# Kernel optimization log

Hardware: AMD Instinct MI355X
Metric: run time of the kernel (lower is better)

Reference implementation:

```python
import jax, jax.numpy as jnp
import numpy as np


def _grid_sample_3d(vol, grid):
    """Trilinear 3D grid_sample, zero padding, align_corners=False (torch default).

    vol:  [B, C, D, H, W]
    grid: [B, P, 3] normalized coords in [-1, 1]; grid[...,0]->W axis,
          grid[...,1]->H axis, grid[...,2]->D axis (torch convention).
    returns [B, C, P]
    """
    B, C, D, H, W = vol.shape
    x = (grid[..., 0] + 1.0) * (W * 0.5) - 0.5
    y = (grid[..., 1] + 1.0) * (H * 0.5) - 0.5
    z = (grid[..., 2] + 1.0) * (D * 0.5) - 0.5
    x0, y0, z0 = jnp.floor(x), jnp.floor(y), jnp.floor(z)
    gather = jax.vmap(lambda v, zz, yy, xx: v[:, zz, yy, xx])  # per-batch gather -> [C, P]
    out = jnp.zeros((B, C, x.shape[1]), vol.dtype)
    for dz in (0.0, 1.0):
        for dy in (0.0, 1.0):
            for dx in (0.0, 1.0):
                xi, yi, zi = x0 + dx, y0 + dy, z0 + dz
                w = (1.0 - jnp.abs(x - xi)) * (1.0 - jnp.abs(y - yi)) * (1.0 - jnp.abs(z - zi))
                valid = (xi >= 0) & (xi < W) & (yi >= 0) & (yi < H) & (zi >= 0) & (zi < D)
                xc = jnp.clip(xi, 0, W - 1).astype(jnp.int32)
                yc = jnp.clip(yi, 0, H - 1).astype(jnp.int32)
                zc = jnp.clip(zi, 0, D - 1).astype(jnp.int32)
                vals = gather(vol, zc, yc, xc)  # [B, C, P]
                out = out + vals * jnp.where(valid, w, 0.0)[:, None, :]
    return out


def _offset_grid(xs, A, Wk):
    """xs: [N,3] sample points; A: [N,3,3]; Wk: [3,K] offset weights.
    Returns [N, K, 3] grid coords ordered (z_feat, y_feat, x_feat) as in the torch code."""
    off = jnp.einsum('nij,jk->nik', A, Wk)  # bmm with repeated weight -> [N,3,K]
    xf = xs[:, 2:3] + off[:, 0, :]
    yf = xs[:, 1:2] + off[:, 1, :]
    zf = xs[:, 0:1] + off[:, 2, :]
    return jnp.stack([zf, yf, xf], axis=-1)


def setup_inputs() -> dict:
    key = jax.random.key(0)
    k1, k2, k3, k4 = jax.random.split(key, 4)
    B, C, D, H, W = 2, 16, 96, 96, 96
    Feats, K = 512, 1024
    inp = jax.random.normal(k1, (B, C, D, H, W), jnp.float32)
    xyz_sample = jax.random.uniform(k2, (B, Feats, 3), jnp.float32, -1.0, 1.0)
    A = jax.random.normal(k3, (B * Feats, 3, 3), jnp.float32) * 0.1
    weight = jax.random.normal(k4, (6, K), jnp.float32) * 0.05  # xyz_off.weight
    return {"input": inp, "xyz_sample": xyz_sample, "A": A, "weight": weight}


def reference(input, xyz_sample, A, weight):
    B, Feats, _ = xyz_sample.shape
    C = input.shape[1]
    K = weight.shape[1]  # 1024
    xs = xyz_sample.reshape(B * Feats, 3)
    g1 = _offset_grid(xs, A, weight[:3]).reshape(B, Feats * K, 3)
    g2 = _offset_grid(xs, A, weight[3:]).reshape(B, Feats * K, 3)
    feats = _grid_sample_3d(input, g1) - _grid_sample_3d(input, g2)  # [B, C, Feats*K]
    return feats.reshape(B, C * Feats, K)
```

## Files before the change

kernel.cpp:

```cpp
#include <hip/hip_runtime.h>
#include <hip/hip_fp16.h>


#define NB 2
#define NC 16
#define NS 96
#define NS3 (NS * NS * NS)
#define FEATS 512
#define NK 1024
#define KSPLIT 2
#define KCHUNK (NK / KSPLIT)
#define PASSES 4

#define RVOX 8

__device__ __forceinline__ int stage_addr(int xg, int yg, int zg, int h) {
  int v = (zg << 6) + (yg << 3) + xg;
  v ^= (yg & 1) << 1;
  return (v << 5) | (((h ^ zg) & 1) << 4);
}

__device__ __forceinline__ unsigned int packh2(float lo, float hi) {
  __half2 h = __halves2half2(__float2half(lo), __float2half(hi));
  return __builtin_bit_cast(unsigned int, h);
}

__device__ __forceinline__ void accpair(unsigned int v, float wt,
                                        float& a0, float& a1) {
  __half2 h = __builtin_bit_cast(__half2, v);
  a0 = fmaf(__low2float(h), wt, a0);
  a1 = fmaf(__high2float(h), wt, a1);
}

__device__ __forceinline__ void acc8(const uint4& u, float wt, float acc[8]) {
  accpair(u.x, wt, acc[0], acc[1]);
  accpair(u.y, wt, acc[2], acc[3]);
  accpair(u.z, wt, acc[4], acc[5]);
  accpair(u.w, wt, acc[6], acc[7]);
}

__device__ __forceinline__ void tri_duo(
    const float* __restrict__ vol, size_t cbase,
    const unsigned char* __restrict__ stage, int duo,
    int ox0, int oy0, int oz0,
    float x, float y, float z, float sgn, float acc[8]) {
  float fx0 = floorf(x), fy0 = floorf(y), fz0 = floorf(z);
  int ix0 = (int)fx0, iy0 = (int)fy0, iz0 = (int)fz0;
  float tx = x - fx0, ty = y - fy0, tz = z - fz0;
  float wxa[2] = {1.0f - tx, tx};
  float wya[2] = {1.0f - ty, ty};
  float wza[2] = {1.0f - tz, tz};

  int lx0 = ix0 - ox0, ly0 = iy0 - oy0, lz0 = iz0 - oz0;
  bool fast = ((unsigned)lx0 < 7u) & ((unsigned)ly0 < 7u) & ((unsigned)lz0 < 7u);

  if (__builtin_expect(fast, 1)) {
#pragma unroll
    for (int dz = 0; dz < 2; dz++) {
      float wz = sgn * wza[dz];
      int vz = lz0 + dz;
#pragma unroll
      for (int dy = 0; dy < 2; dy++) {
        float wzy = wz * wya[dy];
        int vy = ly0 + dy;
#pragma unroll
        for (int dx = 0; dx < 2; dx++) {
          float w = wzy * wxa[dx];
          int vx = lx0 + dx;
          uint4 u = *(const uint4*)(stage + stage_addr(vx, vy, vz, duo));
          acc8(u, w, acc);
        }
      }
    }
  } else {
#pragma unroll
    for (int dz = 0; dz < 2; dz++) {
      int zc = iz0 + dz;
      if ((unsigned)zc >= (unsigned)NS) continue;
#pragma unroll
      for (int dy = 0; dy < 2; dy++) {
        int yc = iy0 + dy;
        if ((unsigned)yc >= (unsigned)NS) continue;
        float wzy = sgn * wza[dz] * wya[dy];
#pragma unroll
        for (int dx = 0; dx < 2; dx++) {
          int xc = ix0 + dx;
          if ((unsigned)xc >= (unsigned)NS) continue;
          float w = wzy * wxa[dx];
          const float* p = vol + cbase + (((size_t)zc * NS + yc) * NS + xc);
#pragma unroll
          for (int c = 0; c < 8; c++)
            acc[c] += w * p[(size_t)c * NS3];
        }
      }
    }
  }
}

__global__ __launch_bounds__(256) void sample_fused(
    const float* __restrict__ vol, const float* __restrict__ xyz,
    const float* __restrict__ A, const float* __restrict__ weight,
    float* __restrict__ out) {
  __shared__ __align__(128) unsigned char stage[RVOX * RVOX * RVOX * 32];

  int bid = blockIdx.x;
  int kseg = bid & (KSPLIT - 1);
  int n = bid >> 1;
  int b = n >> 9;
  int f = n & 511;
  int kbase = kseg * KCHUNK;
  int tid = threadIdx.x;

  const float* Xn = xyz + (size_t)n * 3;
  float bx = (Xn[0] + 1.0f) * 48.0f - 0.5f;
  float by = (Xn[1] + 1.0f) * 48.0f - 0.5f;
  float bz = (Xn[2] + 1.0f) * 48.0f - 0.5f;
  int ox0 = (int)floorf(bx) - 3;
  int oy0 = (int)floorf(by) - 3;
  int oz0 = (int)floorf(bz) - 3;

  int duo = tid & 1;
  int ksub = tid >> 1;

  const float* An = A + (size_t)n * 9;
  float a00 = An[0] * 48.0f, a01 = An[1] * 48.0f, a02 = An[2] * 48.0f;
  float a10 = An[3] * 48.0f, a11 = An[4] * 48.0f, a12 = An[5] * 48.0f;
  float a20 = An[6] * 48.0f, a21 = An[7] * 48.0f, a22 = An[8] * 48.0f;

  size_t vb = (size_t)b * NC * NS3;
#pragma unroll
  for (int j = 0; j < 4; j++) {
    int w = tid + 256 * j;
    int half = w & 1;
    int v = w >> 1;
    int xg = v & 7, yg = (v >> 3) & 7, zg = v >> 6;
    int xc = ox0 + xg, yc = oy0 + yg, zc = oz0 + zg;
    uint4 r = make_uint4(0u, 0u, 0u, 0u);
    if (((unsigned)xc < (unsigned)NS) & ((unsigned)yc < (unsigned)NS) &
        ((unsigned)zc < (unsigned)NS)) {
      const float* p = vol + vb + (size_t)(half * 8) * NS3 +
                       (((size_t)zc * NS + yc) * NS + xc);
      float f0 = p[0];
      float f1 = p[NS3];
      float f2 = p[2 * NS3];
      float f3 = p[3 * NS3];
      float f4 = p[4 * NS3];
      float f5 = p[5 * NS3];
      float f6 = p[6 * NS3];
      float f7 = p[7 * NS3];
      r.x = packh2(f0, f1);
      r.y = packh2(f2, f3);
      r.z = packh2(f4, f5);
      r.w = packh2(f6, f7);
    }
    *(uint4*)(stage + stage_addr(xg, yg, zg, half)) = r;
  }
  __syncthreads();

  size_t cbase = ((size_t)b * NC + duo * 8) * NS3;
  size_t obase = (size_t)b * (NC * FEATS * NK) +
                 (size_t)(duo * 8) * (FEATS * NK) + (size_t)f * NK + kbase;

  float wc[6], wn[6];
#pragma unroll
  for (int q = 0; q < 6; q++) wc[q] = weight[q * NK + kbase + ksub];

  for (int pass = 0; pass < PASSES; pass++) {
    int kl = pass * 128 + ksub;
    if (pass < PASSES - 1) {
#pragma unroll
      for (int q = 0; q < 6; q++) wn[q] = weight[q * NK + kbase + kl + 128];
    }

    float acc[8] = {0.0f, 0.0f, 0.0f, 0.0f, 0.0f, 0.0f, 0.0f, 0.0f};

    {
      float oz = a00 * wc[0] + a01 * wc[1] + a02 * wc[2];
      float oy = a10 * wc[0] + a11 * wc[1] + a12 * wc[2];
      float ox = a20 * wc[0] + a21 * wc[1] + a22 * wc[2];
      tri_duo(vol, cbase, stage, duo, ox0, oy0, oz0, bx + ox, by + oy,
              bz + oz, 1.0f, acc);
    }
    {
      float oz = a00 * wc[3] + a01 * wc[4] + a02 * wc[5];
      float oy = a10 * wc[3] + a11 * wc[4] + a12 * wc[5];
      float ox = a20 * wc[3] + a21 * wc[4] + a22 * wc[5];
      tri_duo(vol, cbase, stage, duo, ox0, oy0, oz0, bx + ox, by + oy,
              bz + oz, -1.0f, acc);
    }

    size_t o = obase + kl;
#pragma unroll
    for (int c = 0; c < 8; c++)
      out[o + (size_t)c * (FEATS * NK)] = acc[c];

#pragma unroll
    for (int q = 0; q < 6; q++) wc[q] = wn[q];
  }
}

extern "C" void kernel_launch(void* const* d_in, const int* in_sizes, int n_in,
                              void* d_out, int out_size, void* d_ws,
                              size_t ws_size, hipStream_t stream) {
  const float* vol    = (const float*)d_in[0];
  const float* xyz    = (const float*)d_in[1];
  const float* A      = (const float*)d_in[2];
  const float* weight = (const float*)d_in[3];
  float* out = (float*)d_out;

  sample_fused<<<NB * FEATS * KSPLIT, 256, 0, stream>>>(vol, xyz, A, weight,
                                                        out);
}
```

Before: 202.0 us.

## Use one 512-thread block per feature with wider staged tile and float2 loads

Drops the K split so each feature point is handled by a single 512-thread block that stages its voxel neighbourhood once instead of twice. The staged region grows to 10x8x8 with an even-aligned x origin, so each staging thread loads two adjacent x voxels as float2 per channel. The XOR bank swizzle in the shared-memory address is removed. This halves the redundant global gathers for staging and widens the loads, at the cost of fewer blocks, a larger block size and possible LDS bank conflicts without the swizzle.

New measurement: 197.6 us. 2.2% less time.

```diff
diff --git a/kernel.cpp b/kernel.cpp
--- a/kernel.cpp
+++ b/kernel.cpp
@@ -8,15 +8,16 @@
 #define NS3 (NS * NS * NS)
 #define FEATS 512
 #define NK 1024
-#define KSPLIT 2
-#define KCHUNK (NK / KSPLIT)
 #define PASSES 4
 
-#define RVOX 8
+#define RX 10
+#define RY 8
+#define RZ 8
+#define NVOX (RX * RY * RZ)
 
 __device__ __forceinline__ int stage_addr(int xg, int yg, int zg, int h) {
-  int v = (zg << 6) + (yg << 3) + xg;
-  v ^= (yg & 1) << 1;
+  int row = (zg << 3) + yg;
+  int v = row * RX + xg;
   return (v << 5) | (((h ^ zg) & 1) << 4);
 }
 
@@ -52,7 +53,9 @@
   float wza[2] = {1.0f - tz, tz};
 
   int lx0 = ix0 - ox0, ly0 = iy0 - oy0, lz0 = iz0 - oz0;
-  bool fast = ((unsigned)lx0 < 7u) & ((unsigned)ly0 < 7u) & ((unsigned)lz0 < 7u);
+  bool fast = ((unsigned)lx0 < (unsigned)(RX - 1)) &
+              ((unsigned)ly0 < (unsigned)(RY - 1)) &
+              ((unsigned)lz0 < (unsigned)(RZ - 1));
 
   if (__builtin_expect(fast, 1)) {
 #pragma unroll
@@ -97,25 +100,22 @@
   }
 }
 
-__global__ __launch_bounds__(256) void sample_fused(
+__global__ __launch_bounds__(512, 4) void sample_fused(
     const float* __restrict__ vol, const float* __restrict__ xyz,
     const float* __restrict__ A, const float* __restrict__ weight,
     float* __restrict__ out) {
-  __shared__ __align__(128) unsigned char stage[RVOX * RVOX * RVOX * 32];
-
-  int bid = blockIdx.x;
-  int kseg = bid & (KSPLIT - 1);
-  int n = bid >> 1;
+  __shared__ __align__(128) unsigned char stage[NVOX * 32];
+
+  int n = blockIdx.x;
   int b = n >> 9;
   int f = n & 511;
-  int kbase = kseg * KCHUNK;
   int tid = threadIdx.x;
 
   const float* Xn = xyz + (size_t)n * 3;
   float bx = (Xn[0] + 1.0f) * 48.0f - 0.5f;
   float by = (Xn[1] + 1.0f) * 48.0f - 0.5f;
   float bz = (Xn[2] + 1.0f) * 48.0f - 0.5f;
-  int ox0 = (int)floorf(bx) - 3;
+  int ox0 = ((int)floorf(bx) - 3) & ~1;
   int oy0 = (int)floorf(by) - 3;
   int oz0 = (int)floorf(bz) - 3;
 
@@ -128,48 +128,56 @@
   float a20 = An[6] * 48.0f, a21 = An[7] * 48.0f, a22 = An[8] * 48.0f;
 
   size_t vb = (size_t)b * NC * NS3;
-#pragma unroll
-  for (int j = 0; j < 4; j++) {
-    int w = tid + 256 * j;
-    int half = w & 1;
-    int v = w >> 1;
-    int xg = v & 7, yg = (v >> 3) & 7, zg = v >> 6;
+  for (int t = tid; t < NVOX; t += 512) {
+    int half = t & 1;
+    int pv = t >> 1;
+    int px = pv % 5;
+    int rowi = pv / 5;
+    int yg = rowi & 7, zg = rowi >> 3;
+    int xg = px << 1;
     int xc = ox0 + xg, yc = oy0 + yg, zc = oz0 + zg;
-    uint4 r = make_uint4(0u, 0u, 0u, 0u);
-    if (((unsigned)xc < (unsigned)NS) & ((unsigned)yc < (unsigned)NS) &
-        ((unsigned)zc < (unsigned)NS)) {
-      const float* p = vol + vb + (size_t)(half * 8) * NS3 +
-                       (((size_t)zc * NS + yc) * NS + xc);
-      float f0 = p[0];
-      float f1 = p[NS3];
-      float f2 = p[2 * NS3];
-      float f3 = p[3 * NS3];
-      float f4 = p[4 * NS3];
-      float f5 = p[5 * NS3];
-      float f6 = p[6 * NS3];
-      float f7 = p[7 * NS3];
-      r.x = packh2(f0, f1);
-      r.y = packh2(f2, f3);
-      r.z = packh2(f4, f5);
-      r.w = packh2(f6, f7);
-    }
-    *(uint4*)(stage + stage_addr(xg, yg, zg, half)) = r;
+    bool rowv = ((unsigned)yc < (unsigned)NS) & ((unsigned)zc < (unsigned)NS);
+    bool v0 = rowv & ((unsigned)xc < (unsigned)NS);
+    bool v1 = rowv & ((unsigned)(xc + 1) < (unsigned)NS);
+    const float* pc = vol + vb + (size_t)(half * 8) * NS3 +
+                      (ptrdiff_t)(((long)zc * NS + yc) * NS + xc);
+    float av[8], bv[8];
+    if (v0 & v1) {
+#pragma unroll
+      for (int c = 0; c < 8; c++) {
+        float2 f2 = *(const float2*)(pc + (size_t)c * NS3);
+        av[c] = f2.x;
+        bv[c] = f2.y;
+      }
+    } else {
+#pragma unroll
+      for (int c = 0; c < 8; c++) {
+        av[c] = v0 ? pc[(size_t)c * NS3] : 0.0f;
+        bv[c] = v1 ? pc[(size_t)c * NS3 + 1] : 0.0f;
+      }
+    }
+    uint4 u0 = make_uint4(packh2(av[0], av[1]), packh2(av[2], av[3]),
+                          packh2(av[4], av[5]), packh2(av[6], av[7]));
+    uint4 u1 = make_uint4(packh2(bv[0], bv[1]), packh2(bv[2], bv[3]),
+                          packh2(bv[4], bv[5]), packh2(bv[6], bv[7]));
+    *(uint4*)(stage + stage_addr(xg, yg, zg, half)) = u0;
+    *(uint4*)(stage + stage_addr(xg + 1, yg, zg, half)) = u1;
   }
   __syncthreads();
 
   size_t cbase = ((size_t)b * NC + duo * 8) * NS3;
   size_t obase = (size_t)b * (NC * FEATS * NK) +
-                 (size_t)(duo * 8) * (FEATS * NK) + (size_t)f * NK + kbase;
+                 (size_t)(duo * 8) * (FEATS * NK) + (size_t)f * NK;
 
   float wc[6], wn[6];
 #pragma unroll
-  for (int q = 0; q < 6; q++) wc[q] = weight[q * NK + kbase + ksub];
+  for (int q = 0; q < 6; q++) wc[q] = weight[q * NK + ksub];
 
   for (int pass = 0; pass < PASSES; pass++) {
-    int kl = pass * 128 + ksub;
+    int kl = pass * 256 + ksub;
     if (pass < PASSES - 1) {
 #pragma unroll
-      for (int q = 0; q < 6; q++) wn[q] = weight[q * NK + kbase + kl + 128];
+      for (int q = 0; q < 6; q++) wn[q] = weight[q * NK + kl + 256];
     }
 
     float acc[8] = {0.0f, 0.0f, 0.0f, 0.0f, 0.0f, 0.0f, 0.0f, 0.0f};
@@ -208,6 +216,5 @@
   const float* weight = (const float*)d_in[3];
   float* out = (float*)d_out;
 
-  sample_fused<<<NB * FEATS * KSPLIT, 256, 0, stream>>>(vol, xyz, A, weight,
-                                                        out);
-}
+  sample_fused<<<NB * FEATS, 512, 0, stream>>>(vol, xyz, A, weight, out);
+}
```
